# Kernel tuning notes

Measured on AMD Instinct MI355X. Metric: run time of the kernel, lower is better.

The kernel has to match this reference:

```python
import jax, jax.numpy as jnp
import numpy as np

ALPHA = 0.2  # leaky relu slope
NEG_BIG = -9e15


def setup_inputs() -> dict:
    key = jax.random.key(0)
    k1, k2, k3, k4 = jax.random.split(key, 4)
    B, N, Fin, Fout = 8, 2048, 128, 128
    h = jax.random.normal(k1, (B, N, Fin), dtype=jnp.float32)
    adj = jax.random.randint(k2, (N, N), 0, 2, dtype=jnp.int32)
    # xavier_uniform with gain=1.414
    limW = 1.414 * np.sqrt(6.0 / (Fin + Fout))
    W = jax.random.uniform(k3, (Fin, Fout), minval=-limW, maxval=limW, dtype=jnp.float32)
    lima = 1.414 * np.sqrt(6.0 / (2 * Fout + 1))
    a = jax.random.uniform(k4, (2 * Fout, 1), minval=-lima, maxval=lima, dtype=jnp.float32)
    return {"h": h, "adj": adj, "W": W, "a": a}


def reference(h, adj, W, a):
    # Wh: [B, N, F]
    Wh = jnp.einsum("bnf,fo->bno", h, W)
    Fout = W.shape[1]
    a1, a2 = a[:Fout, 0], a[Fout:, 0]  # [F], [F]
    # Additive score decomposition (same math as concat trick):
    # e[b,i,j] = leakyrelu(Wh_i . a1 + Wh_j . a2)
    s1 = Wh @ a1  # [B, N] (source/query part)
    s2 = Wh @ a2  # [B, N] (target part)
    e = s1[:, :, None] + s2[:, None, :]  # [B, N, N]
    e = jnp.where(e > 0, e, ALPHA * e)   # leaky relu
    e = jnp.where(adj[None, :, :] > 0, e, NEG_BIG)
    attention = jax.nn.softmax(e, axis=2)  # [B, N, N]
    # dropout is identity in eval mode
    h_prime = jnp.einsum("bij,bjf->bif", attention, Wh)
    return h_prime
```

## Files before the change

kernel.cpp:

```cpp
#include <hip/hip_runtime.h>
#include <hip/hip_bf16.h>
#include <stdint.h>

#define ALPHA 0.2f

typedef __attribute__((ext_vector_type(8))) short bf16x8;
typedef __attribute__((ext_vector_type(4))) float f32x4;

__device__ __forceinline__ short f2bf(float f) {
    union { float f; uint32_t u; } c; c.f = f;
    uint32_t u = c.u + 0x7FFF + ((c.u >> 16) & 1);
    return (short)(u >> 16);
}

__device__ __forceinline__ uint32_t pk_bf16(float lo, float hi) {
    union { float f; uint32_t u; } a, b;
    a.f = lo; b.f = hi;
    return __builtin_amdgcn_perm(b.u + 0x8000u, a.u + 0x8000u, 0x07060302u);
}

__global__ __launch_bounds__(256) void pack_adj_kernel(
        const int* __restrict__ adj, uint8_t* __restrict__ bytes,
        const float* __restrict__ W, short* __restrict__ WTg) {
    int t = blockIdx.x * 256 + threadIdx.x;
    const int4* a4 = reinterpret_cast<const int4*>(adj) + (size_t)t * 2;
    int4 x0 = a4[0], x1 = a4[1];
    uint32_t m = 0;
    m |= (x0.x > 0) ? 1u   : 0u;  m |= (x0.y > 0) ? 2u   : 0u;
    m |= (x0.z > 0) ? 4u   : 0u;  m |= (x0.w > 0) ? 8u   : 0u;
    m |= (x1.x > 0) ? 16u  : 0u;  m |= (x1.y > 0) ? 32u  : 0u;
    m |= (x1.z > 0) ? 64u  : 0u;  m |= (x1.w > 0) ? 128u : 0u;
    bytes[t] = (uint8_t)m;

    if (blockIdx.x < 64) {
        int idx = blockIdx.x * 256 + threadIdx.x;
        int k = idx >> 7, f = idx & 127;
        WTg[f * 128 + k] = f2bf(W[k * 128 + f]);
    }
}

__global__ __launch_bounds__(256) void wh_kernel(
        const float* __restrict__ h, const short* __restrict__ WTg,
        const float* __restrict__ a, short* __restrict__ whT,
        float* __restrict__ s1g, float* __restrict__ s2g) {
    __shared__ float sred[4][2][16];
    __shared__ short tr[4][32][24];

    int tid = threadIdx.x, wid = tid >> 6, lane = tid & 63;
    int q = lane >> 4, n = lane & 15;
    int bb = blockIdx.x & 7;
    int tile = blockIdx.x >> 3;
    int rb = bb * 2048 + tile * 16;
    int row = rb + n;

    f32x4 acc[2] = {};
    #pragma unroll
    for (int kc = 0; kc < 4; ++kc) {
        const float* hp = h + (size_t)row * 128 + kc * 32 + q * 8;
        float4 h0 = reinterpret_cast<const float4*>(hp)[0];
        float4 h1 = reinterpret_cast<const float4*>(hp)[1];
        bf16x8 afrag;
        afrag[0] = f2bf(h0.x); afrag[1] = f2bf(h0.y);
        afrag[2] = f2bf(h0.z); afrag[3] = f2bf(h0.w);
        afrag[4] = f2bf(h1.x); afrag[5] = f2bf(h1.y);
        afrag[6] = f2bf(h1.z); afrag[7] = f2bf(h1.w);
        #pragma unroll
        for (int u = 0; u < 2; ++u) {
            int t = wid * 2 + u;
            bf16x8 bfrag = *reinterpret_cast<const bf16x8*>(
                WTg + (t * 16 + n) * 128 + kc * 32 + q * 8);
            acc[u] = __builtin_amdgcn_mfma_f32_16x16x32_bf16(afrag, bfrag, acc[u], 0, 0, 0);
        }
    }

    float p1[4] = {0.f, 0.f, 0.f, 0.f}, p2[4] = {0.f, 0.f, 0.f, 0.f};
    #pragma unroll
    for (int u = 0; u < 2; ++u) {
        int c = (wid * 2 + u) * 16 + n;
        float a1c = a[c] * 1.442695041f;
        float a2c = a[128 + c] * 1.442695041f;
        #pragma unroll
        for (int r = 0; r < 4; ++r) {
            p1[r] += acc[u][r] * a1c;
            p2[r] += acc[u][r] * a2c;
        }
    }
    #pragma unroll
    for (int d = 1; d < 16; d <<= 1) {
        #pragma unroll
        for (int r = 0; r < 4; ++r) {
            p1[r] += __shfl_xor(p1[r], d);
            p2[r] += __shfl_xor(p2[r], d);
        }
    }
    if (n == 0) {
        #pragma unroll
        for (int r = 0; r < 4; ++r) {
            sred[wid][0][q * 4 + r] = p1[r];
            sred[wid][1][q * 4 + r] = p2[r];
        }
    }

    #pragma unroll
    for (int u = 0; u < 2; ++u)
        #pragma unroll
        for (int r = 0; r < 4; ++r)
            tr[wid][u * 16 + n][q * 4 + r] = f2bf(acc[u][r]);
    __syncthreads();

    if (wid == 0 && lane < 16) {
        float v1 = 0.f, v2 = 0.f;
        #pragma unroll
        for (int v = 0; v < 4; ++v) { v1 += sred[v][0][lane]; v2 += sred[v][1][lane]; }
        s1g[rb + lane] = v1;
        s2g[rb + lane] = v2;
    }

    int jr = rb & 2047;
    int fl = lane & 31, jh = lane >> 5;
    bf16x8 v = *reinterpret_cast<const bf16x8*>(&tr[wid][fl][jh * 8]);
    int f = wid * 32 + fl;
    int t = f >> 4, nn = f & 15;
    int jc = jr >> 5;
    int qg = ((jr & 31) >> 3) + jh;
    *reinterpret_cast<bf16x8*>(
        whT + (size_t)(bb * 64 + jc) * 4096 + t * 512 + qg * 128 + nn * 8) = v;
}

__device__ __forceinline__ void load_nb(const char* gb, int chunk, int lane,
                                        bf16x8* nb) {
    const char* cb = gb + (size_t)chunk * 8192 + lane * 16;
    #pragma unroll
    for (int t = 0; t < 8; ++t)
        nb[t] = *reinterpret_cast<const bf16x8*>(cb + t * 1024);
}

__global__ __launch_bounds__(256, 2) void attn_kernel(
        const short* __restrict__ whT, const float* __restrict__ s1g,
        const float* __restrict__ s2g, const uint8_t* __restrict__ adjb,
        float* __restrict__ out) {
    __shared__ uint32_t mlds[32 * 65];
    __shared__ float s2lds[2048];
    __shared__ float dslds[4][2][16];
    __shared__ f32x4 cbuf[3][16][64];

    int tid = threadIdx.x, wid = tid >> 6, lane = tid & 63;
    int q = lane >> 4, n = lane & 15;
    int b  = blockIdx.x & 7;
    int ib = (blockIdx.x >> 3) * 32;

    float s1A0 = s1g[b * 2048 + ib + n];
    float s1A1 = s1g[b * 2048 + ib + 16 + n];
    const char* gbase = reinterpret_cast<const char*>(whT) + (size_t)b * 524288;

    {
        int r = tid >> 3, sub = tid & 7;
        const uint4* src = reinterpret_cast<const uint4*>(
            adjb + (size_t)(ib + r) * 256 + sub * 32);
        uint4 v0 = src[0], v1 = src[1];
        uint32_t* dst = &mlds[r * 65 + sub * 8];
        dst[0] = v0.x; dst[1] = v0.y; dst[2] = v0.z; dst[3] = v0.w;
        dst[4] = v1.x; dst[5] = v1.y; dst[6] = v1.z; dst[7] = v1.w;
    }
    {
        const float* s2b = s2g + b * 2048;
        float4 v0 = *reinterpret_cast<const float4*>(s2b + tid * 8);
        float4 v1 = *reinterpret_cast<const float4*>(s2b + tid * 8 + 4);
        *reinterpret_cast<float4*>(&s2lds[tid * 8])     = v0;
        *reinterpret_cast<float4*>(&s2lds[tid * 8 + 4]) = v1;
    }
    __syncthreads();

    f32x4 acc0[8] = {}, acc1[8] = {};
    float ds0 = 0.f, ds1 = 0.f;
    int gc0 = wid * 16;
    int mrow0 = n * 65, mrow1 = (16 + n) * 65;

    bf16x8 nbA[8], nbB[8];
    load_nb(gbase, gc0, lane, nbA);

#define PROCESS(C, NB)                                                        \
    {                                                                         \
        int gc = gc0 + (C);                                                   \
        uint32_t mA0 = mlds[mrow0 + gc] >> (q * 8);                           \
        uint32_t mA1 = mlds[mrow1 + gc] >> (q * 8);                           \
        int sb = gc * 32 + q * 8;                                             \
        float4 s2a = *reinterpret_cast<const float4*>(&s2lds[sb]);            \
        float4 s2c = *reinterpret_cast<const float4*>(&s2lds[sb + 4]);        \
        float s2arr[8] = {s2a.x, s2a.y, s2a.z, s2a.w,                         \
                          s2c.x, s2c.y, s2c.z, s2c.w};                        \
        float p0[8], p1[8];                                                   \
        _Pragma("unroll")                                                     \
        for (int j = 0; j < 8; ++j) {                                         \
            float e0 = s1A0 + s2arr[j];                                       \
            e0 = fmaxf(e0, ALPHA * e0);                                       \
            float v0 = ((mA0 >> j) & 1) ? __builtin_amdgcn_exp2f(e0) : 0.0f;  \
            ds0 += v0; p0[j] = v0;                                            \
            float e1 = s1A1 + s2arr[j];                                       \
            e1 = fmaxf(e1, ALPHA * e1);                                       \
            float v1 = ((mA1 >> j) & 1) ? __builtin_amdgcn_exp2f(e1) : 0.0f;  \
            ds1 += v1; p1[j] = v1;                                            \
        }                                                                     \
        union { uint32_t u32[4]; bf16x8 v; } cv0, cv1;                        \
        _Pragma("unroll")                                                     \
        for (int pp = 0; pp < 4; ++pp) {                                      \
            cv0.u32[pp] = pk_bf16(p0[2 * pp], p0[2 * pp + 1]);                \
            cv1.u32[pp] = pk_bf16(p1[2 * pp], p1[2 * pp + 1]);                \
        }                                                                     \
        _Pragma("unroll")                                                     \
        for (int t = 0; t < 8; ++t) {                                         \
            acc0[t] = __builtin_amdgcn_mfma_f32_16x16x32_bf16(                \
                cv0.v, (NB)[t], acc0[t], 0, 0, 0);                            \
            acc1[t] = __builtin_amdgcn_mfma_f32_16x16x32_bf16(                \
                cv1.v, (NB)[t], acc1[t], 0, 0, 0);                            \
        }                                                                     \
    }

    #pragma unroll 1
    for (int cc = 0; cc < 16; cc += 2) {
        load_nb(gbase, gc0 + cc + 1, lane, nbB);
        PROCESS(cc, nbA)
        if (cc + 2 < 16) load_nb(gbase, gc0 + cc + 2, lane, nbA);
        PROCESS(cc + 1, nbB)
    }
#undef PROCESS

    ds0 += __shfl_xor(ds0, 16); ds0 += __shfl_xor(ds0, 32);
    ds1 += __shfl_xor(ds1, 16); ds1 += __shfl_xor(ds1, 32);
    if (q == 0) { dslds[wid][0][n] = ds0; dslds[wid][1][n] = ds1; }

    if (wid != 0) {
        #pragma unroll
        for (int t = 0; t < 8; ++t) {
            cbuf[wid - 1][t][lane]     = acc0[t];
            cbuf[wid - 1][8 + t][lane] = acc1[t];
        }
    }
    __syncthreads();
    if (wid == 0) {
        #pragma unroll
        for (int w = 0; w < 3; ++w)
            #pragma unroll
            for (int t = 0; t < 8; ++t) {
                acc0[t] += cbuf[w][t][lane];
                acc1[t] += cbuf[w][8 + t][lane];
            }

        float dtot0 = dslds[0][0][n] + dslds[1][0][n] + dslds[2][0][n] + dslds[3][0][n];
        float dtot1 = dslds[0][1][n] + dslds[1][1][n] + dslds[2][1][n] + dslds[3][1][n];
        float rd0[4], rd1[4];
        #pragma unroll
        for (int r = 0; r < 4; ++r) {
            rd0[r] = 1.0f / __shfl(dtot0, q * 4 + r);
            rd1[r] = 1.0f / __shfl(dtot1, q * 4 + r);
        }

        size_t ob = ((size_t)b * 2048 + ib) * 128;
        #pragma unroll
        for (int t = 0; t < 8; ++t)
            #pragma unroll
            for (int r = 0; r < 4; ++r) {
                out[ob + (size_t)(q * 4 + r) * 128 + t * 16 + n]        = acc0[t][r] * rd0[r];
                out[ob + (size_t)(16 + q * 4 + r) * 128 + t * 16 + n]   = acc1[t][r] * rd1[r];
            }
    }
}

extern "C" void kernel_launch(void* const* d_in, const int* in_sizes, int n_in,
                              void* d_out, int out_size, void* d_ws, size_t ws_size,
                              hipStream_t stream) {
    const float* h   = (const float*)d_in[0];
    const int*   adj = (const int*)d_in[1];
    const float* W   = (const float*)d_in[2];
    const float* a   = (const float*)d_in[3];
    float* out = (float*)d_out;

    char* ws = (char*)d_ws;
    short* whT = (short*)ws;
    float* s1  = (float*)(ws + 4194304);
    float* s2  = (float*)(ws + 4259840);
    uint8_t* bytes = (uint8_t*)(ws + 4325376);
    short* WTg = (short*)(ws + 4849664);

    pack_adj_kernel<<<2048, 256, 0, stream>>>(adj, bytes, W, WTg);
    wh_kernel<<<1024, 256, 0, stream>>>(h, WTg, a, whT, s1, s2);
    attn_kernel<<<512, 256, 0, stream>>>(whT, s1, s2, bytes, out);
}
```

Before: 104.3 us.

## Distribute final cross-wave reduction across all waves; halve wh_kernel grid with two tiles per block

The attention kernel's epilogue used to have wave 0 sum all 16 accumulator tiles from the other waves and write the whole output while the other three waves sat idle. Now each wave publishes the 12 tiles it does not own to LDS, then reduces, normalizes and stores its own 4 tiles, so the reduction and stores are spread across all waves. The LDS buffer is reshaped to match. Separately, wh_kernel runs two row tiles per block with 512 blocks, which adds an extra barrier between tiles.

After: 104.8 us. No clear change (+0.4%).

```diff
diff --git a/kernel.cpp b/kernel.cpp
--- a/kernel.cpp
+++ b/kernel.cpp
@@ -49,82 +49,88 @@
     int tid = threadIdx.x, wid = tid >> 6, lane = tid & 63;
     int q = lane >> 4, n = lane & 15;
     int bb = blockIdx.x & 7;
-    int tile = blockIdx.x >> 3;
-    int rb = bb * 2048 + tile * 16;
-    int row = rb + n;
-
-    f32x4 acc[2] = {};
+    int tile0 = blockIdx.x >> 3;
+
     #pragma unroll
-    for (int kc = 0; kc < 4; ++kc) {
-        const float* hp = h + (size_t)row * 128 + kc * 32 + q * 8;
-        float4 h0 = reinterpret_cast<const float4*>(hp)[0];
-        float4 h1 = reinterpret_cast<const float4*>(hp)[1];
-        bf16x8 afrag;
-        afrag[0] = f2bf(h0.x); afrag[1] = f2bf(h0.y);
-        afrag[2] = f2bf(h0.z); afrag[3] = f2bf(h0.w);
-        afrag[4] = f2bf(h1.x); afrag[5] = f2bf(h1.y);
-        afrag[6] = f2bf(h1.z); afrag[7] = f2bf(h1.w);
+    for (int t2 = 0; t2 < 2; ++t2) {
+        if (t2) __syncthreads();
+        int tile = tile0 + t2 * 64;
+        int rb = bb * 2048 + tile * 16;
+        int row = rb + n;
+
+        f32x4 acc[2] = {};
+        #pragma unroll
+        for (int kc = 0; kc < 4; ++kc) {
+            const float* hp = h + (size_t)row * 128 + kc * 32 + q * 8;
+            float4 h0 = reinterpret_cast<const float4*>(hp)[0];
+            float4 h1 = reinterpret_cast<const float4*>(hp)[1];
+            bf16x8 afrag;
+            afrag[0] = f2bf(h0.x); afrag[1] = f2bf(h0.y);
+            afrag[2] = f2bf(h0.z); afrag[3] = f2bf(h0.w);
+            afrag[4] = f2bf(h1.x); afrag[5] = f2bf(h1.y);
+            afrag[6] = f2bf(h1.z); afrag[7] = f2bf(h1.w);
+            #pragma unroll
+            for (int u = 0; u < 2; ++u) {
+                int t = wid * 2 + u;
+                bf16x8 bfrag = *reinterpret_cast<const bf16x8*>(
+                    WTg + (t * 16 + n) * 128 + kc * 32 + q * 8);
+                acc[u] = __builtin_amdgcn_mfma_f32_16x16x32_bf16(afrag, bfrag, acc[u], 0, 0, 0);
+            }
+        }
+
+        float p1[4] = {0.f, 0.f, 0.f, 0.f}, p2[4] = {0.f, 0.f, 0.f, 0.f};
         #pragma unroll
         for (int u = 0; u < 2; ++u) {
-            int t = wid * 2 + u;
-            bf16x8 bfrag = *reinterpret_cast<const bf16x8*>(
-                WTg + (t * 16 + n) * 128 + kc * 32 + q * 8);
-            acc[u] = __builtin_amdgcn_mfma_f32_16x16x32_bf16(afrag, bfrag, acc[u], 0, 0, 0);
-        }
-    }
-
-    float p1[4] = {0.f, 0.f, 0.f, 0.f}, p2[4] = {0.f, 0.f, 0.f, 0.f};
-    #pragma unroll
-    for (int u = 0; u < 2; ++u) {
-        int c = (wid * 2 + u) * 16 + n;
-        float a1c = a[c] * 1.442695041f;
-        float a2c = a[128 + c] * 1.442695041f;
-        #pragma unroll
-        for (int r = 0; r < 4; ++r) {
-            p1[r] += acc[u][r] * a1c;
-            p2[r] += acc[u][r] * a2c;
-        }
-    }
-    #pragma unroll
-    for (int d = 1; d < 16; d <<= 1) {
-        #pragma unroll
-        for (int r = 0; r < 4; ++r) {
-            p1[r] += __shfl_xor(p1[r], d);
-            p2[r] += __shfl_xor(p2[r], d);
-        }
-    }
-    if (n == 0) {
-        #pragma unroll
-        for (int r = 0; r < 4; ++r) {
-            sred[wid][0][q * 4 + r] = p1[r];
-            sred[wid][1][q * 4 + r] = p2[r];
-        }
-    }
-
-    #pragma unroll
-    for (int u = 0; u < 2; ++u)
-        #pragma unroll
-        for (int r = 0; r < 4; ++r)
-            tr[wid][u * 16 + n][q * 4 + r] = f2bf(acc[u][r]);
-    __syncthreads();
-
-    if (wid == 0 && lane < 16) {
-        float v1 = 0.f, v2 = 0.f;
-        #pragma unroll
-        for (int v = 0; v < 4; ++v) { v1 += sred[v][0][lane]; v2 += sred[v][1][lane]; }
-        s1g[rb + lane] = v1;
-        s2g[rb + lane] = v2;
-    }
-
-    int jr = rb & 2047;
-    int fl = lane & 31, jh = lane >> 5;
-    bf16x8 v = *reinterpret_cast<const bf16x8*>(&tr[wid][fl][jh * 8]);
-    int f = wid * 32 + fl;
-    int t = f >> 4, nn = f & 15;
-    int jc = jr >> 5;
-    int qg = ((jr & 31) >> 3) + jh;
-    *reinterpret_cast<bf16x8*>(
-        whT + (size_t)(bb * 64 + jc) * 4096 + t * 512 + qg * 128 + nn * 8) = v;
+            int c = (wid * 2 + u) * 16 + n;
+            float a1c = a[c] * 1.442695041f;
+            float a2c = a[128 + c] * 1.442695041f;
+            #pragma unroll
+            for (int r = 0; r < 4; ++r) {
+                p1[r] += acc[u][r] * a1c;
+                p2[r] += acc[u][r] * a2c;
+            }
+        }
+        #pragma unroll
+        for (int d = 1; d < 16; d <<= 1) {
+            #pragma unroll
+            for (int r = 0; r < 4; ++r) {
+                p1[r] += __shfl_xor(p1[r], d);
+                p2[r] += __shfl_xor(p2[r], d);
+            }
+        }
+        if (n == 0) {
+            #pragma unroll
+            for (int r = 0; r < 4; ++r) {
+                sred[wid][0][q * 4 + r] = p1[r];
+                sred[wid][1][q * 4 + r] = p2[r];
+            }
+        }
+
+        #pragma unroll
+        for (int u = 0; u < 2; ++u)
+            #pragma unroll
+            for (int r = 0; r < 4; ++r)
+                tr[wid][u * 16 + n][q * 4 + r] = f2bf(acc[u][r]);
+        __syncthreads();
+
+        if (wid == 0 && lane < 16) {
+            float v1 = 0.f, v2 = 0.f;
+            #pragma unroll
+            for (int v = 0; v < 4; ++v) { v1 += sred[v][0][lane]; v2 += sred[v][1][lane]; }
+            s1g[rb + lane] = v1;
+            s2g[rb + lane] = v2;
+        }
+
+        int jr = rb & 2047;
+        int fl = lane & 31, jh = lane >> 5;
+        bf16x8 v = *reinterpret_cast<const bf16x8*>(&tr[wid][fl][jh * 8]);
+        int f = wid * 32 + fl;
+        int t = f >> 4, nn = f & 15;
+        int jc = jr >> 5;
+        int qg = ((jr & 31) >> 3) + jh;
+        *reinterpret_cast<bf16x8*>(
+            whT + (size_t)(bb * 64 + jc) * 4096 + t * 512 + qg * 128 + nn * 8) = v;
+    }
 }
 
 __device__ __forceinline__ void load_nb(const char* gb, int chunk, int lane,
@@ -142,7 +148,7 @@
     __shared__ uint32_t mlds[32 * 65];
     __shared__ float s2lds[2048];
     __shared__ float dslds[4][2][16];
-    __shared__ f32x4 cbuf[3][16][64];
+    __shared__ f32x4 cbuf[4][12][64];
 
     int tid = threadIdx.x, wid = tid >> 6, lane = tid & 63;
     int q = lane >> 4, n = lane & 15;
@@ -229,40 +235,56 @@
     ds1 += __shfl_xor(ds1, 16); ds1 += __shfl_xor(ds1, 32);
     if (q == 0) { dslds[wid][0][n] = ds0; dslds[wid][1][n] = ds1; }
 
-    if (wid != 0) {
-        #pragma unroll
-        for (int t = 0; t < 8; ++t) {
-            cbuf[wid - 1][t][lane]     = acc0[t];
-            cbuf[wid - 1][8 + t][lane] = acc1[t];
+    {
+        int j = 0;
+        #pragma unroll
+        for (int s = 0; s < 16; ++s) {
+            if ((s >> 2) != wid) {
+                cbuf[wid][j][lane] = (s < 8) ? acc0[s] : acc1[s - 8];
+                ++j;
+            }
         }
     }
     __syncthreads();
-    if (wid == 0) {
-        #pragma unroll
-        for (int w = 0; w < 3; ++w)
-            #pragma unroll
-            for (int t = 0; t < 8; ++t) {
-                acc0[t] += cbuf[w][t][lane];
-                acc1[t] += cbuf[w][8 + t][lane];
-            }
-
-        float dtot0 = dslds[0][0][n] + dslds[1][0][n] + dslds[2][0][n] + dslds[3][0][n];
-        float dtot1 = dslds[0][1][n] + dslds[1][1][n] + dslds[2][1][n] + dslds[3][1][n];
-        float rd0[4], rd1[4];
-        #pragma unroll
-        for (int r = 0; r < 4; ++r) {
-            rd0[r] = 1.0f / __shfl(dtot0, q * 4 + r);
-            rd1[r] = 1.0f / __shfl(dtot1, q * 4 + r);
-        }
-
-        size_t ob = ((size_t)b * 2048 + ib) * 128;
-        #pragma unroll
-        for (int t = 0; t < 8; ++t)
-            #pragma unroll
-            for (int r = 0; r < 4; ++r) {
-                out[ob + (size_t)(q * 4 + r) * 128 + t * 16 + n]        = acc0[t][r] * rd0[r];
-                out[ob + (size_t)(16 + q * 4 + r) * 128 + t * 16 + n]   = acc1[t][r] * rd1[r];
-            }
+
+    {
+        int rgown = wid >> 1;
+        float dtot = dslds[0][rgown][n] + dslds[1][rgown][n]
+                   + dslds[2][rgown][n] + dslds[3][rgown][n];
+        float rd[4];
+        #pragma unroll
+        for (int r = 0; r < 4; ++r)
+            rd[r] = 1.0f / __shfl(dtot, q * 4 + r);
+
+        size_t ob = ((size_t)b * 2048 + ib + rgown * 16) * 128;
+
+#define FINISH(K, ACCARR, TBASE)                                              \
+        {                                                                     \
+            int s = wid * 4 + (K);                           \
+            int t = (TBASE) + (K);                     \
+            f32x4 v = (ACCARR)[t];                                            \
+            _Pragma("unroll")                                                 \
+            for (int w2 = 0; w2 < 4; ++w2) {                                  \
+                if (w2 != wid) {                                              \
+                    int j2 = s - (((s >> 2) > w2) ? 4 : 0);                   \
+                    v += cbuf[w2][j2][lane];                                  \
+                }                                                             \
+            }                                                                 \
+            _Pragma("unroll")                                                 \
+            for (int r = 0; r < 4; ++r)                                       \
+                out[ob + (size_t)(q * 4 + r) * 128 + t * 16 + n] = v[r] * rd[r]; \
+        }
+
+        if (wid == 0) {
+            FINISH(0, acc0, 0) FINISH(1, acc0, 0) FINISH(2, acc0, 0) FINISH(3, acc0, 0)
+        } else if (wid == 1) {
+            FINISH(0, acc0, 4) FINISH(1, acc0, 4) FINISH(2, acc0, 4) FINISH(3, acc0, 4)
+        } else if (wid == 2) {
+            FINISH(0, acc1, 0) FINISH(1, acc1, 0) FINISH(2, acc1, 0) FINISH(3, acc1, 0)
+        } else {
+            FINISH(0, acc1, 4) FINISH(1, acc1, 4) FINISH(2, acc1, 4) FINISH(3, acc1, 4)
+        }
+#undef FINISH
     }
 }
 
@@ -283,6 +305,6 @@
     short* WTg = (short*)(ws + 4849664);
 
     pack_adj_kernel<<<2048, 256, 0, stream>>>(adj, bytes, W, WTg);
-    wh_kernel<<<1024, 256, 0, stream>>>(h, WTg, a, whT, s1, s2);
+    wh_kernel<<<512, 256, 0, stream>>>(h, WTg, a, whT, s1, s2);
     attn_kernel<<<512, 256, 0, stream>>>(whT, s1, s2, bytes, out);
 }
```
